# Kernel optimization log

Hardware: AMD Instinct MI355X
Metric: run time of the kernel (lower is better)

## Reference

```python
import jax, jax.numpy as jnp
import numpy as np

B, C, R, M, N = 8, 16, 16, 512, 512
ASYM = 1e-3


def _rot(a, z):
    # torch: r = (a*z).diff(-1) = a1*z1 - a0*z0 ; i = (a*z[...,[1,0]]).sum(-1) = a0*z1 + a1*z0
    r = a[..., 1] * z[..., 1] - a[..., 0] * z[..., 0]
    i = a[..., 0] * z[..., 1] + a[..., 1] * z[..., 0]
    return jnp.stack([r, i], axis=-1)


def _cmatmul(a, b):
    # complex matmul on trailing [..., P, Q, 2] x [..., Q, S, 2] (equivalent to the A/B einsum trick)
    ar, ai = a[..., 0], a[..., 1]
    br, bi = b[..., 0], b[..., 1]
    return jnp.stack([ar @ br - ai @ bi, ar @ bi + ai @ br], axis=-1)


def setup_inputs() -> dict:
    key = jax.random.key(0)
    ks = jax.random.split(key, 14)
    rn = lambda k, s, sc=1.0: jax.random.normal(k, s, dtype=jnp.float32) * sc
    rot_init = lambda k1, k2: jnp.concatenate(
        [1.0 + rn(k1, (1, C, 1, 1, 1), ASYM), rn(k2, (1, C, 1, 1, 1), ASYM)], axis=-1)
    return {
        "x": rn(ks[0], (B, C)),
        "weights_i": rn(ks[1], (1, 1, M, M, 2), 1.0 / np.log(M * M)),
        "weights_j": rn(ks[2], (1, 1, N, N, 2), 1.0 / np.log(N * N)),
        "weights_base": rn(ks[3], (1, 1, M, N, 2), 1.0 / np.log(M * N)),
        "translate_base": rn(ks[4], (1, C, 1, 1, 2), ASYM),
        "rotate_base": rot_init(ks[5], ks[6]),
        "translate_dynamic": rn(ks[7], (1, C, 1, 1, 2), ASYM),
        "rotate_dynamic": rot_init(ks[8], ks[9]),
        "mod_i": rn(ks[10], (1, C, R, M, 2), 1.0 / np.log(R * M)),
        "mod_j": rn(ks[11], (1, C, R, N, 2)),
        "inversions": -1.0 + rn(ks[12], (1, C, 1, 1, 2), ASYM),
        "mod_transforms": rn(ks[13], (4, C, 2 * C), np.sqrt(2.0 / (3 * C))),
    }


def reference(x, weights_i, weights_j, weights_base, translate_base, rotate_base,
              translate_dynamic, rotate_dynamic, mod_i, mod_j, inversions, mod_transforms):
    Bx = x.shape[0]
    # NOTE: the original computes a rotated/translated `weights` from weights_base,
    # translate_base, rotate_base that is never used afterwards (dead code) -> omitted.
    t = jnp.einsum('bc,kcl->bkl', x, mod_transforms)          # [B,4,2C]
    t = t.reshape(Bx, 4, C, 1, 1, 2)
    # low-rank modulation factors, per component, rotated by dynamic transforms
    mi = _rot(mod_i + t[:, 0], t[:, 1])                        # [B,C,R,M,2]
    mj = _rot(mod_j + t[:, 2], t[:, 3])                        # [B,C,R,N,2]
    # inversion-rotate mod_i then sum over components
    mi = _rot(mi, inversions).sum(axis=1, keepdims=True)       # [B,1,R,M,2]
    # "division-like" inversion for mod_j then sum over components
    denom = (mj * mj).sum(axis=-1, keepdims=True)
    r = (inversions * mj).sum(axis=-1, keepdims=True) / denom
    i = (inversions[..., 0:1] * mj[..., 1:2] - inversions[..., 1:2] * mj[..., 0:1]) / denom
    mj = jnp.concatenate([r, i], axis=-1).sum(axis=1, keepdims=True)  # [B,1,R,N,2]
    # complex outer-product modulation: [B,1,M,R] @ [B,1,R,N] -> [B,1,M,N,2]
    mod = _cmatmul(jnp.swapaxes(mi, -3, -2), mj)
    mr = mod[..., 0]
    mr = (mr - mr.mean(axis=(-2, -1), keepdims=True)) / jnp.std(mr, axis=(-2, -1), ddof=1, keepdims=True)
    mod = jnp.stack([mr, mod[..., 1]], axis=-1)
    # modulate base weights (componentwise, not complex mult)
    wd = weights_base + weights_base * mod                     # [B,1,M,N,2]
    # cross-mixing complex matmuls
    wd = _cmatmul(jnp.swapaxes(wd, -3, -2), weights_i)         # [B,1,N,M,2]
    wd = _cmatmul(jnp.swapaxes(wd, -3, -2), weights_j)         # [B,1,M,N,2]
    # per-component dynamic translate + rotate, sum components, take real part
    wd = wd + translate_dynamic                                # [B,C,M,N,2]
    wd = _rot(wd, rotate_dynamic).sum(axis=1)[..., 0]          # [B,M,N]
    return wd
```

## Files before the change

kernel.cpp:

```cpp
#include <hip/hip_runtime.h>
#include <hip/hip_bf16.h>
#include <math.h>


#define WS_STATS   1296
#define WS_MIS     4096
#define WS_MJS     135168
#define WS_BASET   266240
#define WS_A2      790528
#define WS_B5T     1052672
#define WS_G1X     1314816
#define WS_B2T     3411968
#define WS_GP      7606272
#define WS_CS      7737344

typedef __attribute__((ext_vector_type(8))) short short8;
typedef __attribute__((ext_vector_type(4))) float f32x4;

__device__ __forceinline__ unsigned short f2bf(float f) {
    unsigned int u = __float_as_uint(f);
    u = (u + 0x7FFFu + ((u >> 16) & 1u)) >> 16;
    return (unsigned short)u;
}
__device__ __forceinline__ unsigned int pack2bf(float a, float b) {
    return (unsigned int)f2bf(a) | ((unsigned int)f2bf(b) << 16);
}
__device__ __forceinline__ void load_lds16(const unsigned short* g, unsigned short* l) {
    __builtin_amdgcn_global_load_lds((const __attribute__((address_space(1))) unsigned int*)g,
                                     (__attribute__((address_space(3))) unsigned int*)l, 16, 0, 0);
}

__global__ void k_trans(const float* __restrict__ Wi, const float* __restrict__ Wj,
                        const float* __restrict__ base, const float* __restrict__ rd,
                        float* __restrict__ ws) {
    __shared__ float2 tile[32][33];
    int mode = blockIdx.z;
    int bx = blockIdx.x, by = blockIdx.y;
    int tx = threadIdx.x & 31, ty = threadIdx.x >> 5;
    const float* src = (mode == 0) ? Wi : (mode == 1) ? Wj : base;
    for (int i = 0; i < 4; i++) {
        int rIn = by * 32 + ty + i * 8;
        int cIn = bx * 32 + tx;
        tile[ty + i * 8][tx] = *(const float2*)(src + ((size_t)rIn * 512 + cIn) * 2);
    }
    __syncthreads();
    if (mode == 0) {
        unsigned int* A2u = (unsigned int*)(ws + WS_A2);
        for (int i = 0; i < 4; i++) {
            int rOut = bx * 32 + ty + i * 8;
            int cOut = by * 32 + tx;
            float2 v = tile[tx][ty + i * 8];
            A2u[(size_t)rOut * 512 + cOut] = pack2bf(v.x, v.y);
        }
    } else if (mode == 1) {
        float ar = 0.f, ai = 0.f;
        for (int c = 0; c < 16; c++) { ar -= rd[2 * c]; ai -= rd[2 * c + 1]; }
        unsigned int* B5u = (unsigned int*)(ws + WS_B5T);
        for (int i = 0; i < 4; i++) {
            int rOut = bx * 32 + ty + i * 8;
            int cOut = by * 32 + tx;
            float2 v = tile[tx][ty + i * 8];
            float wr = ar * v.x - ai * v.y;
            float wi = ar * v.y + ai * v.x;
            B5u[(size_t)rOut * 512 + cOut] = pack2bf(wr, -wi);
        }
    } else {
        float* baseT = ws + WS_BASET;
        for (int i = 0; i < 4; i++) {
            int rOut = bx * 32 + ty + i * 8;
            int cOut = by * 32 + tx;
            *(float2*)(baseT + ((size_t)rOut * 512 + cOut) * 2) = tile[tx][ty + i * 8];
        }
    }
}

__global__ void k_mimj(const float* __restrict__ x, const float* __restrict__ mt,
                       const float* __restrict__ inv, const float* __restrict__ mod_i,
                       const float* __restrict__ mod_j, float* __restrict__ ws) {
    __shared__ float tb[128];
    __shared__ float deS[32];
    int blk = blockIdx.x;
    bool isMi = blk < 256;
    int id = (isMi ? blk : blk - 256) * 256 + threadIdx.x;
    int b = id >> 13, rm = id & 8191;
    int tid = threadIdx.x;
    if (tid < 128) {
        int k = tid >> 5, l = tid & 31;
        float s = 0.f;
        for (int c = 0; c < 16; c++) s += x[b * 16 + c] * mt[(k * 16 + c) * 32 + l];
        tb[tid] = s;
    }
    __syncthreads();
    if (tid < 16) {
        float i0 = inv[2 * tid], i1 = inv[2 * tid + 1];
        float z0 = tb[32 + 2 * tid], z1 = tb[32 + 2 * tid + 1];
        deS[2 * tid]     = i0 * z0 + i1 * z1;
        deS[2 * tid + 1] = i0 * z1 - i1 * z0;
    }
    __syncthreads();
    if (isMi) {
        float acc0 = 0.f, acc1 = 0.f;
        for (int c = 0; c < 16; c++) {
            const float* p = mod_i + (((size_t)c * 8192) + rm) * 2;
            float A0 = p[0] + tb[2 * c], A1 = p[1] + tb[2 * c + 1];
            float d = deS[2 * c], e = deS[2 * c + 1];
            acc0 += d * A0 - e * A1;
            acc1 += e * A0 + d * A1;
        }
        float* dst = ws + WS_MIS + ((size_t)b * 8192 + rm) * 2;
        dst[0] = acc0; dst[1] = acc1;
    } else {
        float acc0 = 0.f, acc1 = 0.f;
        for (int c = 0; c < 16; c++) {
            const float* p = mod_j + (((size_t)c * 8192) + rm) * 2;
            float A0 = p[0] + tb[64 + 2 * c], A1 = p[1] + tb[64 + 2 * c + 1];
            float z0 = tb[96 + 2 * c], z1 = tb[96 + 2 * c + 1];
            float w0 = -z0 * A0 + z1 * A1;
            float w1 =  z1 * A0 + z0 * A1;
            float i0 = inv[2 * c], i1 = inv[2 * c + 1];
            float den = w0 * w0 + w1 * w1;
            acc0 += (i0 * w0 + i1 * w1) / den;
            acc1 += (i0 * w1 - i1 * w0) / den;
        }
        float* dst = ws + WS_MJS + ((size_t)b * 8192 + rm) * 2;
        dst[0] = acc0; dst[1] = acc1;
    }
}

__global__ __launch_bounds__(256) void k_gram1(float* __restrict__ ws) {
    __shared__ float2 Vs[16][66];
    __shared__ float2 Us[16][66];
    int ch = blockIdx.x, b = blockIdx.y, tid = threadIdx.x;
    int r = tid >> 4, r2 = tid & 15;
    const float2* V = (const float2*)(ws + WS_MIS + (size_t)b * 16384);
    const float2* U = (const float2*)(ws + WS_MJS + (size_t)b * 16384);
    int c0 = ch * 64;
    for (int p = 0; p < 4; p++) {
        int f = tid + p * 256;
        int rr = f >> 6, mm = f & 63;
        Vs[rr][mm] = V[rr * 512 + c0 + mm];
        Us[rr][mm] = U[rr * 512 + c0 + mm];
    }
    __syncthreads();
    float Svr = 0, Svi = 0, Tvr = 0, Tvi = 0;
    float Sur = 0, Sui = 0, Tur = 0, Tui = 0;
    float ar = 0, ai = 0, br = 0, bi = 0;
    for (int mm = 0; mm < 64; mm++) {
        float2 v1 = Vs[r][mm], v2 = Vs[r2][mm];
        float2 u1 = Us[r][mm], u2 = Us[r2][mm];
        Svr += v1.x * v2.x - v1.y * v2.y;  Svi += v1.x * v2.y + v1.y * v2.x;
        Tvr += v1.x * v2.x + v1.y * v2.y;  Tvi += v1.y * v2.x - v1.x * v2.y;
        Sur += u1.x * u2.x - u1.y * u2.y;  Sui += u1.x * u2.y + u1.y * u2.x;
        Tur += u1.x * u2.x + u1.y * u2.y;  Tui += u1.y * u2.x - u1.x * u2.y;
        if (r2 == 0) { ar += v1.x; ai += v1.y; br += u1.x; bi += u1.y; }
    }
    float4* g4 = (float4*)(ws + WS_GP + (((size_t)b * 8 + ch) * 256 + tid) * 8);
    g4[0] = make_float4(Svr, Svi, Tvr, Tvi);
    g4[1] = make_float4(Sur, Sui, Tur, Tui);
    if (r2 == 0)
        *(float4*)(ws + WS_CS + (((size_t)b * 8 + ch) * 16 + r) * 4) =
            make_float4(ar, ai, br, bi);
}

__global__ __launch_bounds__(256) void k_gram2(float* __restrict__ ws) {
    __shared__ float red[256];
    __shared__ float red2[16];
    int b = blockIdx.x, tid = threadIdx.x;
    float Svr = 0, Svi = 0, Tvr = 0, Tvi = 0;
    float Sur = 0, Sui = 0, Tur = 0, Tui = 0;
    for (int ch = 0; ch < 8; ch++) {
        const float4* g4 = (const float4*)(ws + WS_GP + (((size_t)b * 8 + ch) * 256 + tid) * 8);
        float4 a0 = g4[0], a1 = g4[1];
        Svr += a0.x; Svi += a0.y; Tvr += a0.z; Tvi += a0.w;
        Sur += a1.x; Sui += a1.y; Tur += a1.z; Tui += a1.w;
    }
    red[tid] = (Sur * Svr - Sui * Svi) + (Tur * Tvr - Tui * Tvi);
    if (tid < 16) {
        float ar = 0, ai = 0, br = 0, bi = 0;
        for (int ch = 0; ch < 8; ch++) {
            float4 c = *(const float4*)(ws + WS_CS + (((size_t)b * 8 + ch) * 16 + tid) * 4);
            ar += c.x; ai += c.y; br += c.z; bi += c.w;
        }
        red2[tid] = br * ar - bi * ai;
    }
    __syncthreads();
    for (int s = 128; s > 0; s >>= 1) {
        if (tid < s) red[tid] += red[tid + s];
        __syncthreads();
    }
    if (tid == 0) {
        float msum = 0.f;
        for (int i = 0; i < 16; i++) msum += red2[i];
        double MN = 262144.0;
        double mu = (double)msum / MN;
        double sumsq = 0.5 * (double)red[0];
        double var = (sumsq - MN * mu * mu) / (MN - 1.0);
        if (var < 1e-30) var = 1e-30;
        float* stats = ws + WS_STATS;
        stats[b * 2] = (float)mu;
        stats[b * 2 + 1] = (float)(1.0 / sqrt(var));
    }
}

__global__ __launch_bounds__(256) void k_bmod(float* __restrict__ ws) {
    const float* mi_s  = ws + WS_MIS;
    const float* mj_s  = ws + WS_MJS;
    const float* baseT = ws + WS_BASET;
    const float* stats = ws + WS_STATS;
    unsigned int* B2T  = (unsigned int*)(ws + WS_B2T);
    int mt = blockIdx.x, nt = blockIdx.y, b = blockIdx.z;
    __shared__ float Ns[16][128];
    __shared__ float Ms[16][128];
    int tid = threadIdx.x, tx = tid & 15, ty = tid >> 4;
    const float* Nb = mj_s + (size_t)b * 16384;
    const float* Mb = mi_s + (size_t)b * 16384;
    int n0 = nt * 64, m0 = mt * 64;
    for (int i = 0; i < 4; i++) {
        int flat = tid + i * 256;
        int col = flat & 63, r = flat >> 6;
        float2 sa = *(const float2*)(Nb + ((size_t)r * 512 + n0 + col) * 2);
        Ns[r][col * 2] = sa.x; Ns[r][col * 2 + 1] = sa.y;
        float2 sb = *(const float2*)(Mb + ((size_t)r * 512 + m0 + col) * 2);
        Ms[r][col * 2] = sb.x; Ms[r][col * 2 + 1] = sb.y;
    }
    __syncthreads();
    float cr[4][4] = {}, ci[4][4] = {};
    for (int r = 0; r < 16; r++) {
        float nr[4], ni[4], mr[4], mi_[4];
        for (int i = 0; i < 4; i++) { nr[i] = Ns[r][(ty * 4 + i) * 2]; ni[i] = Ns[r][(ty * 4 + i) * 2 + 1]; }
        for (int j = 0; j < 4; j++) { mr[j] = Ms[r][(tx + j * 16) * 2]; mi_[j] = Ms[r][(tx + j * 16) * 2 + 1]; }
        for (int i = 0; i < 4; i++)
            for (int j = 0; j < 4; j++) {
                cr[i][j] += nr[i] * mr[j] - ni[i] * mi_[j];
                ci[i][j] += nr[i] * mi_[j] + ni[i] * mr[j];
            }
    }
    float mu = stats[b * 2], rstd = stats[b * 2 + 1];
    unsigned int* Bb = B2T + (size_t)b * 524288;
    for (int i = 0; i < 4; i++) {
        int n = n0 + ty * 4 + i;
        for (int j = 0; j < 4; j++) {
            int m = m0 + tx + j * 16;
            float2 bs = *(const float2*)(baseT + ((size_t)n * 512 + m) * 2);
            float wr = bs.x * (1.f + (cr[i][j] - mu) * rstd);
            float wi = bs.y * (1.f + ci[i][j]);
            Bb[(size_t)(2 * n) * 512 + m]     = pack2bf(wr, -wi);
            Bb[(size_t)(2 * n + 1) * 512 + m] = pack2bf(wi, wr);
        }
    }
}

template <int TM, int TN, bool OUT_BF16>
__global__ __launch_bounds__(256) void k_gemm(const unsigned short* __restrict__ Aall,
                                              const unsigned short* __restrict__ BTall,
                                              void* __restrict__ Call,
                                              const float* __restrict__ td,
                                              const float* __restrict__ rd,
                                              size_t a_bs, size_t bt_bs, size_t c_bs,
                                              int ngl) {
    constexpr int K = 1024;
    constexpr int IT = TM / 32, JT = TN / 32;
    constexpr int SMAB = (TM + TN) * 64;
    constexpr int SMC = OUT_BF16 ? TM * (TN + 8) : 0;
    constexpr int SMEMN = SMAB > SMC ? SMAB : SMC;
    __shared__ __align__(16) unsigned short smem[SMEMN];
    unsigned short* As = smem;
    unsigned short* Bs = smem + TM * 64;

    const int tid = threadIdx.x;
    const int b = blockIdx.z;
    const unsigned short* A  = Aall  + (size_t)b * a_bs;
    const unsigned short* BT = BTall + (size_t)b * bt_bs;
    const int mBase = blockIdx.y * TM;
    const int nBase = blockIdx.x * TN;
    const int wave = tid >> 6, lane = tid & 63;
    const int wm = wave >> 1, wn = wave & 1;
    const int l15 = lane & 15, q = lane >> 4;

    f32x4 acc[IT][JT];
    for (int i = 0; i < IT; i++)
        for (int j = 0; j < JT; j++) acc[i][j] = (f32x4)0.f;

    for (int k0 = 0; k0 < K; k0 += 64) {
#pragma unroll
        for (int p = 0; p < TM / 32; p++) {
            int flat = tid + p * 256;
            int r = flat >> 3, c = flat & 7;
            int gc = (c ^ (r & 7)) << 3;
            load_lds16(A + (size_t)(mBase + r) * K + k0 + gc, &As[flat << 3]);
        }
#pragma unroll
        for (int p = 0; p < TN / 32; p++) {
            int flat = tid + p * 256;
            int r = flat >> 3, c = flat & 7;
            int gc = (c ^ (r & 7)) << 3;
            load_lds16(BT + (size_t)(nBase + r) * K + k0 + gc, &Bs[flat << 3]);
        }
        __syncthreads();
#pragma unroll
        for (int ks = 0; ks < 2; ks++) {
            short8 af[IT], bfr[JT];
#pragma unroll
            for (int t = 0; t < IT; t++) {
                int ra = wm * (TM / 2) + t * 16 + l15;
                int ja = (ks * 4 + q) ^ (ra & 7);
                af[t] = *(const short8*)&As[ra * 64 + ja * 8];
            }
#pragma unroll
            for (int t = 0; t < JT; t++) {
                int rb = wn * (TN / 2) + t * 16 + l15;
                int jb = (ks * 4 + q) ^ (rb & 7);
                bfr[t] = *(const short8*)&Bs[rb * 64 + jb * 8];
            }
#pragma unroll
            for (int i = 0; i < IT; i++)
#pragma unroll
                for (int j = 0; j < JT; j++)
                    acc[i][j] = __builtin_amdgcn_mfma_f32_16x16x32_bf16(af[i], bfr[j], acc[i][j], 0, 0, 0);
        }
        __syncthreads();
    }

    if constexpr (OUT_BF16) {
        unsigned short* Cs = smem;
#pragma unroll
        for (int i = 0; i < IT; i++) {
            int row0 = wm * (TM / 2) + i * 16 + q * 4;
#pragma unroll
            for (int j = 0; j < JT; j++) {
                int col = wn * (TN / 2) + j * 16 + l15;
#pragma unroll
                for (int r = 0; r < 4; r++)
                    Cs[(row0 + r) * (TN + 8) + col] = f2bf(acc[i][j][r]);
            }
        }
        __syncthreads();
        unsigned short* C = (unsigned short*)Call + (size_t)b * c_bs;
#pragma unroll
        for (int p = 0; p < TM * TN / 2048; p++) {
            int flat = tid + p * 256;
            int r = flat / (TN / 8), c = flat % (TN / 8);
            short8 v = *(const short8*)&Cs[r * (TN + 8) + c * 8];
            *(short8*)(C + (size_t)(mBase + r) * ngl + nBase + c * 8) = v;
        }
    } else {
        float CC = 0.f;
        for (int c = 0; c < 16; c++) CC += td[2 * c + 1] * rd[2 * c + 1] - td[2 * c] * rd[2 * c];
        float* C = (float*)Call + (size_t)b * c_bs;
#pragma unroll
        for (int i = 0; i < IT; i++) {
            int row0 = mBase + wm * (TM / 2) + i * 16 + q * 4;
#pragma unroll
            for (int j = 0; j < JT; j++) {
                int col = nBase + wn * (TN / 2) + j * 16 + l15;
#pragma unroll
                for (int r = 0; r < 4; r++)
                    C[(size_t)(row0 + r) * ngl + col] = acc[i][j][r] + CC;
            }
        }
    }
}

extern "C" void kernel_launch(void* const* d_in, const int* in_sizes, int n_in,
                              void* d_out, int out_size, void* d_ws, size_t ws_size,
                              hipStream_t stream) {
    const float* x    = (const float*)d_in[0];
    const float* Wi   = (const float*)d_in[1];
    const float* Wj   = (const float*)d_in[2];
    const float* base = (const float*)d_in[3];
    const float* td   = (const float*)d_in[6];
    const float* rd   = (const float*)d_in[7];
    const float* modi = (const float*)d_in[8];
    const float* modj = (const float*)d_in[9];
    const float* inv  = (const float*)d_in[10];
    const float* mt   = (const float*)d_in[11];
    float* ws  = (float*)d_ws;
    float* out = (float*)d_out;

    unsigned short* A2  = (unsigned short*)(ws + WS_A2);
    unsigned short* B5T = (unsigned short*)(ws + WS_B5T);
    unsigned short* B2T = (unsigned short*)(ws + WS_B2T);
    unsigned short* G1X = (unsigned short*)(ws + WS_G1X);

    k_trans<<<dim3(16, 16, 3), 256, 0, stream>>>(Wi, Wj, base, rd, ws);
    k_mimj<<<512, 256, 0, stream>>>(x, mt, inv, modi, modj, ws);
    k_gram1<<<dim3(8, 8), 256, 0, stream>>>(ws);
    k_gram2<<<8, 256, 0, stream>>>(ws);
    k_bmod<<<dim3(8, 8, 8), 256, 0, stream>>>(ws);
    k_gemm<128, 128, true><<<dim3(8, 4, 8), 256, 0, stream>>>(
        A2, B2T, (void*)G1X, td, rd, (size_t)0, (size_t)1048576, (size_t)524288, 1024);
    k_gemm<128, 128, false><<<dim3(4, 4, 8), 256, 0, stream>>>(
        G1X, B5T, (void*)out, td, rd, (size_t)524288, (size_t)0, (size_t)262144, 512);
}
```

Measured before the change: 150.9 us.

## Fuse front kernels, double-buffer GEMM LDS stages, shrink second GEMM tile

Merges the transpose/convert kernel and the mi/mj modulation kernel into one launch with a block-range dispatch, saving one kernel launch and its serialization gap. The GEMM kernel now double-buffers its LDS tiles, issuing the next k-step's global-to-LDS loads before computing the current one, with one barrier per iteration. The second GEMM switches to a 64x128 tile to double its block count. The price is twice the LDS per block, which can lower occupancy, plus a larger fused kernel with branchy dispatch.

Measured after the change: 136.6 us. -9.5%, faster.

```diff
diff --git a/kernel.cpp b/kernel.cpp
--- a/kernel.cpp
+++ b/kernel.cpp
@@ -30,100 +30,103 @@
                                      (__attribute__((address_space(3))) unsigned int*)l, 16, 0, 0);
 }
 
-__global__ void k_trans(const float* __restrict__ Wi, const float* __restrict__ Wj,
+__global__ void k_front(const float* __restrict__ Wi, const float* __restrict__ Wj,
                         const float* __restrict__ base, const float* __restrict__ rd,
-                        float* __restrict__ ws) {
-    __shared__ float2 tile[32][33];
-    int mode = blockIdx.z;
-    int bx = blockIdx.x, by = blockIdx.y;
-    int tx = threadIdx.x & 31, ty = threadIdx.x >> 5;
-    const float* src = (mode == 0) ? Wi : (mode == 1) ? Wj : base;
-    for (int i = 0; i < 4; i++) {
-        int rIn = by * 32 + ty + i * 8;
-        int cIn = bx * 32 + tx;
-        tile[ty + i * 8][tx] = *(const float2*)(src + ((size_t)rIn * 512 + cIn) * 2);
-    }
-    __syncthreads();
-    if (mode == 0) {
-        unsigned int* A2u = (unsigned int*)(ws + WS_A2);
+                        const float* __restrict__ x, const float* __restrict__ mt,
+                        const float* __restrict__ inv, const float* __restrict__ mod_i,
+                        const float* __restrict__ mod_j, float* __restrict__ ws) {
+    __shared__ __align__(16) char shmem[32 * 33 * 8];
+    int blk = blockIdx.x;
+    int tid = threadIdx.x;
+    if (blk < 768) {
+        float2(*tile)[33] = (float2(*)[33])shmem;
+        int mode = blk >> 8;
+        int idx = blk & 255;
+        int bx = idx & 15, by = idx >> 4;
+        int tx = tid & 31, ty = tid >> 5;
+        const float* src = (mode == 0) ? Wi : (mode == 1) ? Wj : base;
         for (int i = 0; i < 4; i++) {
-            int rOut = bx * 32 + ty + i * 8;
-            int cOut = by * 32 + tx;
-            float2 v = tile[tx][ty + i * 8];
-            A2u[(size_t)rOut * 512 + cOut] = pack2bf(v.x, v.y);
-        }
-    } else if (mode == 1) {
-        float ar = 0.f, ai = 0.f;
-        for (int c = 0; c < 16; c++) { ar -= rd[2 * c]; ai -= rd[2 * c + 1]; }
-        unsigned int* B5u = (unsigned int*)(ws + WS_B5T);
-        for (int i = 0; i < 4; i++) {
-            int rOut = bx * 32 + ty + i * 8;
-            int cOut = by * 32 + tx;
-            float2 v = tile[tx][ty + i * 8];
-            float wr = ar * v.x - ai * v.y;
-            float wi = ar * v.y + ai * v.x;
-            B5u[(size_t)rOut * 512 + cOut] = pack2bf(wr, -wi);
+            int rIn = by * 32 + ty + i * 8;
+            int cIn = bx * 32 + tx;
+            tile[ty + i * 8][tx] = *(const float2*)(src + ((size_t)rIn * 512 + cIn) * 2);
+        }
+        __syncthreads();
+        if (mode == 0) {
+            unsigned int* A2u = (unsigned int*)(ws + WS_A2);
+            for (int i = 0; i < 4; i++) {
+                int rOut = bx * 32 + ty + i * 8;
+                int cOut = by * 32 + tx;
+                float2 v = tile[tx][ty + i * 8];
+                A2u[(size_t)rOut * 512 + cOut] = pack2bf(v.x, v.y);
+            }
+        } else if (mode == 1) {
+            float ar = 0.f, ai = 0.f;
+            for (int c = 0; c < 16; c++) { ar -= rd[2 * c]; ai -= rd[2 * c + 1]; }
+            unsigned int* B5u = (unsigned int*)(ws + WS_B5T);
+            for (int i = 0; i < 4; i++) {
+                int rOut = bx * 32 + ty + i * 8;
+                int cOut = by * 32 + tx;
+                float2 v = tile[tx][ty + i * 8];
+                float wr = ar * v.x - ai * v.y;
+                float wi = ar * v.y + ai * v.x;
+                B5u[(size_t)rOut * 512 + cOut] = pack2bf(wr, -wi);
+            }
+        } else {
+            float* baseT = ws + WS_BASET;
+            for (int i = 0; i < 4; i++) {
+                int rOut = bx * 32 + ty + i * 8;
+                int cOut = by * 32 + tx;
+                *(float2*)(baseT + ((size_t)rOut * 512 + cOut) * 2) = tile[tx][ty + i * 8];
+            }
         }
     } else {
-        float* baseT = ws + WS_BASET;
-        for (int i = 0; i < 4; i++) {
-            int rOut = bx * 32 + ty + i * 8;
-            int cOut = by * 32 + tx;
-            *(float2*)(baseT + ((size_t)rOut * 512 + cOut) * 2) = tile[tx][ty + i * 8];
-        }
-    }
-}
-
-__global__ void k_mimj(const float* __restrict__ x, const float* __restrict__ mt,
-                       const float* __restrict__ inv, const float* __restrict__ mod_i,
-                       const float* __restrict__ mod_j, float* __restrict__ ws) {
-    __shared__ float tb[128];
-    __shared__ float deS[32];
-    int blk = blockIdx.x;
-    bool isMi = blk < 256;
-    int id = (isMi ? blk : blk - 256) * 256 + threadIdx.x;
-    int b = id >> 13, rm = id & 8191;
-    int tid = threadIdx.x;
-    if (tid < 128) {
-        int k = tid >> 5, l = tid & 31;
-        float s = 0.f;
-        for (int c = 0; c < 16; c++) s += x[b * 16 + c] * mt[(k * 16 + c) * 32 + l];
-        tb[tid] = s;
-    }
-    __syncthreads();
-    if (tid < 16) {
-        float i0 = inv[2 * tid], i1 = inv[2 * tid + 1];
-        float z0 = tb[32 + 2 * tid], z1 = tb[32 + 2 * tid + 1];
-        deS[2 * tid]     = i0 * z0 + i1 * z1;
-        deS[2 * tid + 1] = i0 * z1 - i1 * z0;
-    }
-    __syncthreads();
-    if (isMi) {
-        float acc0 = 0.f, acc1 = 0.f;
-        for (int c = 0; c < 16; c++) {
-            const float* p = mod_i + (((size_t)c * 8192) + rm) * 2;
-            float A0 = p[0] + tb[2 * c], A1 = p[1] + tb[2 * c + 1];
-            float d = deS[2 * c], e = deS[2 * c + 1];
-            acc0 += d * A0 - e * A1;
-            acc1 += e * A0 + d * A1;
-        }
-        float* dst = ws + WS_MIS + ((size_t)b * 8192 + rm) * 2;
-        dst[0] = acc0; dst[1] = acc1;
-    } else {
-        float acc0 = 0.f, acc1 = 0.f;
-        for (int c = 0; c < 16; c++) {
-            const float* p = mod_j + (((size_t)c * 8192) + rm) * 2;
-            float A0 = p[0] + tb[64 + 2 * c], A1 = p[1] + tb[64 + 2 * c + 1];
-            float z0 = tb[96 + 2 * c], z1 = tb[96 + 2 * c + 1];
-            float w0 = -z0 * A0 + z1 * A1;
-            float w1 =  z1 * A0 + z0 * A1;
-            float i0 = inv[2 * c], i1 = inv[2 * c + 1];
-            float den = w0 * w0 + w1 * w1;
-            acc0 += (i0 * w0 + i1 * w1) / den;
-            acc1 += (i0 * w1 - i1 * w0) / den;
-        }
-        float* dst = ws + WS_MJS + ((size_t)b * 8192 + rm) * 2;
-        dst[0] = acc0; dst[1] = acc1;
+        float* tb = (float*)shmem;
+        float* deS = (float*)shmem + 128;
+        int blk2 = blk - 768;
+        bool isMi = blk2 < 256;
+        int id = (isMi ? blk2 : blk2 - 256) * 256 + tid;
+        int b = id >> 13, rm = id & 8191;
+        if (tid < 128) {
+            int k = tid >> 5, l = tid & 31;
+            float s = 0.f;
+            for (int c = 0; c < 16; c++) s += x[b * 16 + c] * mt[(k * 16 + c) * 32 + l];
+            tb[tid] = s;
+        }
+        __syncthreads();
+        if (tid < 16) {
+            float i0 = inv[2 * tid], i1 = inv[2 * tid + 1];
+            float z0 = tb[32 + 2 * tid], z1 = tb[32 + 2 * tid + 1];
+            deS[2 * tid]     = i0 * z0 + i1 * z1;
+            deS[2 * tid + 1] = i0 * z1 - i1 * z0;
+        }
+        __syncthreads();
+        if (isMi) {
+            float acc0 = 0.f, acc1 = 0.f;
+            for (int c = 0; c < 16; c++) {
+                const float* p = mod_i + (((size_t)c * 8192) + rm) * 2;
+                float A0 = p[0] + tb[2 * c], A1 = p[1] + tb[2 * c + 1];
+                float d = deS[2 * c], e = deS[2 * c + 1];
+                acc0 += d * A0 - e * A1;
+                acc1 += e * A0 + d * A1;
+            }
+            float* dst = ws + WS_MIS + ((size_t)b * 8192 + rm) * 2;
+            dst[0] = acc0; dst[1] = acc1;
+        } else {
+            float acc0 = 0.f, acc1 = 0.f;
+            for (int c = 0; c < 16; c++) {
+                const float* p = mod_j + (((size_t)c * 8192) + rm) * 2;
+                float A0 = p[0] + tb[64 + 2 * c], A1 = p[1] + tb[64 + 2 * c + 1];
+                float z0 = tb[96 + 2 * c], z1 = tb[96 + 2 * c + 1];
+                float w0 = -z0 * A0 + z1 * A1;
+                float w1 =  z1 * A0 + z0 * A1;
+                float i0 = inv[2 * c], i1 = inv[2 * c + 1];
+                float den = w0 * w0 + w1 * w1;
+                acc0 += (i0 * w0 + i1 * w1) / den;
+                acc1 += (i0 * w1 - i1 * w0) / den;
+            }
+            float* dst = ws + WS_MJS + ((size_t)b * 8192 + rm) * 2;
+            dst[0] = acc0; dst[1] = acc1;
+        }
     }
 }
 
@@ -259,13 +262,12 @@
                                               size_t a_bs, size_t bt_bs, size_t c_bs,
                                               int ngl) {
     constexpr int K = 1024;
+    constexpr int NK = K / 64;
     constexpr int IT = TM / 32, JT = TN / 32;
-    constexpr int SMAB = (TM + TN) * 64;
+    constexpr int STG = (TM + TN) * 64;
     constexpr int SMC = OUT_BF16 ? TM * (TN + 8) : 0;
-    constexpr int SMEMN = SMAB > SMC ? SMAB : SMC;
+    constexpr int SMEMN = (2 * STG > SMC) ? 2 * STG : SMC;
     __shared__ __align__(16) unsigned short smem[SMEMN];
-    unsigned short* As = smem;
-    unsigned short* Bs = smem + TM * 64;
 
     const int tid = threadIdx.x;
     const int b = blockIdx.z;
@@ -281,7 +283,9 @@
     for (int i = 0; i < IT; i++)
         for (int j = 0; j < JT; j++) acc[i][j] = (f32x4)0.f;
 
-    for (int k0 = 0; k0 < K; k0 += 64) {
+    auto stage = [&](int k0, int buf) {
+        unsigned short* As = smem + buf * STG;
+        unsigned short* Bs = As + TM * 64;
 #pragma unroll
         for (int p = 0; p < TM / 32; p++) {
             int flat = tid + p * 256;
@@ -296,7 +300,14 @@
             int gc = (c ^ (r & 7)) << 3;
             load_lds16(BT + (size_t)(nBase + r) * K + k0 + gc, &Bs[flat << 3]);
         }
-        __syncthreads();
+    };
+
+    stage(0, 0);
+    for (int kt = 0; kt < NK; kt++) {
+        __syncthreads();
+        if (kt + 1 < NK) stage((kt + 1) * 64, (kt + 1) & 1);
+        const unsigned short* As = smem + (kt & 1) * STG;
+        const unsigned short* Bs = As + TM * 64;
 #pragma unroll
         for (int ks = 0; ks < 2; ks++) {
             short8 af[IT], bfr[JT];
@@ -318,10 +329,10 @@
                 for (int j = 0; j < JT; j++)
                     acc[i][j] = __builtin_amdgcn_mfma_f32_16x16x32_bf16(af[i], bfr[j], acc[i][j], 0, 0, 0);
         }
-        __syncthreads();
     }
 
     if constexpr (OUT_BF16) {
+        __syncthreads();
         unsigned short* Cs = smem;
 #pragma unroll
         for (int i = 0; i < IT; i++) {
@@ -382,13 +393,12 @@
     unsigned short* B2T = (unsigned short*)(ws + WS_B2T);
     unsigned short* G1X = (unsigned short*)(ws + WS_G1X);
 
-    k_trans<<<dim3(16, 16, 3), 256, 0, stream>>>(Wi, Wj, base, rd, ws);
-    k_mimj<<<512, 256, 0, stream>>>(x, mt, inv, modi, modj, ws);
+    k_front<<<1280, 256, 0, stream>>>(Wi, Wj, base, rd, x, mt, inv, modi, modj, ws);
     k_gram1<<<dim3(8, 8), 256, 0, stream>>>(ws);
     k_gram2<<<8, 256, 0, stream>>>(ws);
     k_bmod<<<dim3(8, 8, 8), 256, 0, stream>>>(ws);
     k_gemm<128, 128, true><<<dim3(8, 4, 8), 256, 0, stream>>>(
         A2, B2T, (void*)G1X, td, rd, (size_t)0, (size_t)1048576, (size_t)524288, 1024);
-    k_gemm<128, 128, false><<<dim3(4, 4, 8), 256, 0, stream>>>(
+    k_gemm<64, 128, false><<<dim3(4, 8, 8), 256, 0, stream>>>(
         G1X, B5T, (void*)out, td, rd, (size_t)524288, (size_t)0, (size_t)262144, 512);
 }
```
